# Performance work log

Measured on AMD Instinct MI355X. Metric: run time of the kernel, lower is better.

The kernel has to match this reference:

```python
import jax, jax.numpy as jnp
import numpy as np

N_NODES = 100000
N_EDGES = 1600000
IN_H = 18        # n_rw + 2
NHID_STR = 256
OUT_H = 11       # max(1, int(18/64*40))
NCLASS = 40


def gcn_conv(x, edge_index, W, b, num_nodes):
    """PyG GCNConv: add self-loops, symmetric norm, gather-matmul-scatter."""
    x = x @ W  # [N, out]
    loops = jnp.arange(num_nodes, dtype=edge_index.dtype)
    src = jnp.concatenate([edge_index[0], loops])
    dst = jnp.concatenate([edge_index[1], loops])
    deg = jax.ops.segment_sum(jnp.ones_like(dst, dtype=x.dtype), dst,
                              num_segments=num_nodes)
    dinv = jnp.where(deg > 0, jax.lax.rsqrt(deg), 0.0)
    norm = dinv[src] * dinv[dst]  # [E+N]
    msgs = x[src] * norm[:, None]  # gather + scale
    out = jax.ops.segment_sum(msgs, dst, num_segments=num_nodes)
    return out + b


def setup_inputs() -> dict:
    key = jax.random.key(0)
    ks = jax.random.split(key, 10)
    stc_enc = jax.random.normal(ks[0], (N_NODES, IN_H), dtype=jnp.float32)
    edge_index = jax.random.randint(ks[1], (2, N_EDGES), 0, N_NODES, dtype=jnp.int64)
    emb_a = jax.random.normal(ks[2], (N_NODES, NCLASS), dtype=jnp.float32)
    # Glorot-ish params
    W1 = jax.random.normal(ks[3], (IN_H, NHID_STR), dtype=jnp.float32) / np.sqrt(IN_H)
    b1 = jnp.zeros((NHID_STR,), dtype=jnp.float32)
    W2 = jax.random.normal(ks[4], (NHID_STR, OUT_H), dtype=jnp.float32) / np.sqrt(NHID_STR)
    b2 = jnp.zeros((OUT_H,), dtype=jnp.float32)
    Wc = jax.random.normal(ks[5], (NCLASS + OUT_H, NCLASS), dtype=jnp.float32) / np.sqrt(NCLASS + OUT_H)
    bc = jnp.zeros((NCLASS,), dtype=jnp.float32)
    return {"stc_enc": stc_enc, "edge_index": edge_index, "emb_a": emb_a,
            "W1": W1, "b1": b1, "W2": W2, "b2": b2, "Wc": Wc, "bc": bc}


def reference(stc_enc, edge_index, emb_a, W1, b1, W2, b2, Wc, bc):
    # eval mode: F.dropout(training=False) is identity
    h = gcn_conv(stc_enc, edge_index, W1, b1, N_NODES)
    h = gcn_conv(h, edge_index, W2, b2, N_NODES)
    emb_b = jax.nn.relu(h)
    emb = jnp.concatenate([emb_a, emb_b], axis=-1)  # [N, nclass+out_h]
    return emb @ Wc + bc
```

## Files before the change

### kernel.cpp

```cpp
#include <hip/hip_runtime.h>

#define N_NODES 100000
#define N_EDGES 1600000
#define IN_H 18
#define OUT_H 11
#define NCLASS 40
#define NHID 256

#define BBITS 9
#define BINS 512
#define NB 196
#define NBLK 800
#define CHUNK 2000
#define SRC_MASK 0x1FFFF

typedef float    vfloat4 __attribute__((ext_vector_type(4)));
typedef unsigned vuint2  __attribute__((ext_vector_type(2)));

__device__ __forceinline__ float bflo(unsigned u) { return __uint_as_float(u << 16); }
__device__ __forceinline__ float bfhi(unsigned u) { return __uint_as_float(u & 0xFFFF0000u); }
__device__ __forceinline__ unsigned bfr(float x) {
    unsigned u = __float_as_uint(x);
    return (u + 0x7FFFu + ((u >> 16) & 1u)) >> 16;
}
__device__ __forceinline__ unsigned bfpack(float a, float b) { return bfr(a) | (bfr(b) << 16); }
__device__ __forceinline__ float4 bfunpack4(uint2 w) {
    return make_float4(bflo(w.x), bfhi(w.x), bflo(w.y), bfhi(w.y));
}

__global__ void k_hist(const int* __restrict__ dst, int* __restrict__ bh, int E) {
    __shared__ int h[NB];
    int t = threadIdx.x;
    if (t < NB) h[t] = 0;
    __syncthreads();
    const int4* d4 = (const int4*)(dst + blockIdx.x * CHUNK);
    for (int i = t; i < CHUNK / 4; i += blockDim.x) {
        int4 w = d4[i];
        atomicAdd(&h[w.x >> BBITS], 1);
        atomicAdd(&h[w.y >> BBITS], 1);
        atomicAdd(&h[w.z >> BBITS], 1);
        atomicAdd(&h[w.w >> BBITS], 1);
    }
    __syncthreads();
    if (t < NB) bh[t * NBLK + blockIdx.x] = h[t];
}

__global__ void k_btot(const int* __restrict__ bh, int* __restrict__ btot) {
    __shared__ int s[256];
    int b = blockIdx.x, t = threadIdx.x;
    int sum = 0;
    for (int k = t; k < NBLK; k += 256) sum += bh[b * NBLK + k];
    s[t] = sum;
    __syncthreads();
    for (int off = 128; off > 0; off >>= 1) {
        if (t < off) s[t] += s[t + off];
        __syncthreads();
    }
    if (t == 0) btot[b] = s[0];
}

__global__ __launch_bounds__(1024) void k_boff(int* __restrict__ bh,
                                               const int* __restrict__ btot,
                                               int* __restrict__ bstart) {
    __shared__ int s0[1024], s1[1024];
    __shared__ int bt0[256], bt1[256];
    int b = blockIdx.x, t = threadIdx.x;
    if (t < 256) bt0[t] = (t < NB) ? btot[t] : 0;
    __syncthreads();
    int* c0 = bt0; int* c1 = bt1;
    for (int off = 1; off < 256; off <<= 1) {
        if (t < 256) c1[t] = c0[t] + ((t >= off) ? c0[t - off] : 0);
        __syncthreads();
        int* tmp = c0; c0 = c1; c1 = tmp;
    }
    int base = c0[b] - btot[b];
    if (t == 0) {
        bstart[b] = base;
        if (b == 0) bstart[NB] = N_EDGES;
    }
    int v = (t < NBLK) ? bh[b * NBLK + t] : 0;
    s0[t] = v;
    __syncthreads();
    int* c = s0; int* n = s1;
    for (int off = 1; off < 1024; off <<= 1) {
        n[t] = c[t] + ((t >= off) ? c[t - off] : 0);
        __syncthreads();
        int* tmp = c; c = n; n = tmp;
    }
    if (t < NBLK) bh[b * NBLK + t] = c[t] - v + base;
}

__global__ void k_bucket(const int* __restrict__ ei, const int* __restrict__ bh,
                         unsigned int* __restrict__ packed, int E) {
    __shared__ int cur[NB];
    int t = threadIdx.x;
    if (t < NB) cur[t] = bh[t * NBLK + blockIdx.x];
    __syncthreads();
    int base = blockIdx.x * CHUNK;
    const int4* s4 = (const int4*)(ei + base);
    const int4* d4 = (const int4*)(ei + E + base);
    for (int i = t; i < CHUNK / 4; i += blockDim.x) {
        int4 s = s4[i];
        int4 d = d4[i];
        int sl;
        sl = atomicAdd(&cur[d.x >> BBITS], 1);
        packed[sl] = ((unsigned)(d.x & (BINS - 1)) << 17) | (unsigned)s.x;
        sl = atomicAdd(&cur[d.y >> BBITS], 1);
        packed[sl] = ((unsigned)(d.y & (BINS - 1)) << 17) | (unsigned)s.y;
        sl = atomicAdd(&cur[d.z >> BBITS], 1);
        packed[sl] = ((unsigned)(d.z & (BINS - 1)) << 17) | (unsigned)s.z;
        sl = atomicAdd(&cur[d.w >> BBITS], 1);
        packed[sl] = ((unsigned)(d.w & (BINS - 1)) << 17) | (unsigned)s.w;
    }
}

__global__ void k_w12(const float* __restrict__ W1, const float* __restrict__ b1,
                      const float* __restrict__ W2,
                      float* __restrict__ W12, float* __restrict__ bb) {
    int t = threadIdx.x;
    if (t < IN_H * OUT_H) {
        int i = t / OUT_H, j = t % OUT_H;
        float s = 0.f;
        for (int k = 0; k < NHID; ++k) s += W1[i * NHID + k] * W2[k * OUT_H + j];
        W12[t] = s;
    } else if (t < IN_H * OUT_H + OUT_H) {
        int j = t - IN_H * OUT_H;
        float s = 0.f;
        for (int k = 0; k < NHID; ++k) s += b1[k] * W2[k * OUT_H + j];
        bb[j] = s;
    }
}

__global__ __launch_bounds__(1024)
void k_sort(const unsigned int* __restrict__ packed, const int* __restrict__ bstart,
            const float* __restrict__ X, const float* __restrict__ W12g,
            int* __restrict__ col, int* __restrict__ rowptr,
            float* __restrict__ dinv, unsigned int* __restrict__ Pp) {
    __shared__ int hist[BINS];
    __shared__ int s0[BINS], s1[BINS];
    __shared__ int cur[BINS];
    __shared__ float sW[IN_H * OUT_H];
    int b = blockIdx.x, t = threadIdx.x;
    int beg = bstart[b], end = bstart[b + 1];
    if (t < BINS) hist[t] = 0;
    if (t >= BINS && t < BINS + IN_H * OUT_H) sW[t - BINS] = W12g[t - BINS];
    __syncthreads();
    for (int i = beg + t; i < end; i += blockDim.x)
        atomicAdd(&hist[packed[i] >> 17], 1);
    __syncthreads();
    if (t < BINS) s0[t] = hist[t];
    __syncthreads();
    int* c = s0; int* n = s1;
    for (int off = 1; off < BINS; off <<= 1) {
        if (t < BINS) n[t] = c[t] + ((t >= off) ? c[t - off] : 0);
        __syncthreads();
        int* tmp = c; c = n; n = tmp;
    }
    if (t < BINS) {
        int excl = c[t] - hist[t];
        int gbase = beg + excl;
        cur[t] = gbase;
        int node = (b << BBITS) + t;
        if (node <= N_NODES) rowptr[node] = gbase;
        if (node < N_NODES)  dinv[node] = rsqrtf((float)(hist[t] + 1));
    }
    __syncthreads();
    for (int i = beg + t; i < end; i += blockDim.x) {
        unsigned p = packed[i];
        int slot = atomicAdd(&cur[p >> 17], 1);
        col[slot] = (int)(p & SRC_MASK);
    }
    int node = (b << BBITS) + t;
    if (t < BINS && node < N_NODES) {
        float dv = rsqrtf((float)(hist[t] + 1));
        float x[IN_H];
        const float2* xr = (const float2*)(X + (size_t)node * IN_H);
        #pragma unroll
        for (int k = 0; k < IN_H / 2; ++k) {
            float2 cc = xr[k];
            x[2 * k] = cc.x; x[2 * k + 1] = cc.y;
        }
        float pf[12];
        #pragma unroll
        for (int j = 0; j < OUT_H; ++j) {
            float s = 0.f;
            #pragma unroll
            for (int k = 0; k < IN_H; ++k) s += x[k] * sW[k * OUT_H + j];
            pf[j] = dv * s;
        }
        pf[11] = dv;
        uint4* pw = (uint4*)(Pp + (size_t)node * 8);
        pw[0] = make_uint4(bfpack(pf[0], pf[1]), bfpack(pf[2], pf[3]),
                           bfpack(pf[4], pf[5]), bfpack(pf[6], pf[7]));
        pw[1] = make_uint4(bfpack(pf[8], pf[9]), bfpack(pf[10], pf[11]), 0u, 0u);
    }
}

__global__ void k_gather1(const int* __restrict__ rowptr, const int* __restrict__ col,
                          const float* __restrict__ dinv, const unsigned int* __restrict__ Pp,
                          unsigned int* __restrict__ Z1p, float* __restrict__ r, int n) {
    int g = blockIdx.x * blockDim.x + threadIdx.x;
    int v = g >> 3;
    if (v >= n) return;
    int sub  = (g >> 2) & 1;
    int lane = g & 3;
    int beg = rowptr[v], end = rowptr[v + 1];
    int half = (end - beg) >> 1;
    int qbeg = beg + (sub ? half : 0);
    int qend = sub ? end : beg + half;
    float4 acc = make_float4(0.f, 0.f, 0.f, 0.f);
    const uint2* P2 = (const uint2*)Pp;
    int e = qbeg;
    if (e + 3 < qend) {
        int i0 = col[e], i1 = col[e + 1], i2 = col[e + 2], i3 = col[e + 3];
        e += 4;
        for (;;) {
            bool more = (e + 3 < qend);
            int j0, j1, j2, j3;
            if (more) {
                j0 = col[e]; j1 = col[e + 1]; j2 = col[e + 2]; j3 = col[e + 3];
            }
            float4 a0 = bfunpack4(P2[(size_t)i0 * 4 + lane]);
            float4 a1 = bfunpack4(P2[(size_t)i1 * 4 + lane]);
            float4 a2 = bfunpack4(P2[(size_t)i2 * 4 + lane]);
            float4 a3 = bfunpack4(P2[(size_t)i3 * 4 + lane]);
            acc.x += a0.x + a1.x + a2.x + a3.x;
            acc.y += a0.y + a1.y + a2.y + a3.y;
            acc.z += a0.z + a1.z + a2.z + a3.z;
            acc.w += a0.w + a1.w + a2.w + a3.w;
            if (!more) break;
            i0 = j0; i1 = j1; i2 = j2; i3 = j3;
            e += 4;
        }
    }
    for (; e < qend; ++e) {
        float4 a = bfunpack4(P2[(size_t)col[e] * 4 + lane]);
        acc.x += a.x; acc.y += a.y; acc.z += a.z; acc.w += a.w;
    }
    if (!sub) {
        float4 a = bfunpack4(P2[(size_t)v * 4 + lane]);
        acc.x += a.x; acc.y += a.y; acc.z += a.z; acc.w += a.w;
    }
    acc.x += __shfl_xor(acc.x, 4, 8);
    acc.y += __shfl_xor(acc.y, 4, 8);
    acc.z += __shfl_xor(acc.z, 4, 8);
    acc.w += __shfl_xor(acc.w, 4, 8);
    if (!sub) {
        float dd = dinv[v];
        float s2 = dd * dd;
        vuint2 z;
        z.x = bfpack(s2 * acc.x, s2 * acc.y);
        z.y = bfpack(s2 * acc.z, s2 * acc.w);
        __builtin_nontemporal_store(z, (vuint2*)Z1p + (size_t)v * 4 + lane);
        if (lane == 2) __builtin_nontemporal_store(dd * acc.w, r + v);
    }
}

__global__ void k_g2d(const int* __restrict__ rowptr, const int* __restrict__ col,
                      const float* __restrict__ dinv, const unsigned int* __restrict__ Z1p,
                      const float* __restrict__ r, const float* __restrict__ bbg,
                      const float* __restrict__ b2g, const float* __restrict__ emb_a,
                      const float* __restrict__ Wc, const float* __restrict__ bc,
                      float* __restrict__ out, int n) {
    __shared__ float sWc[(NCLASS + OUT_H) * NCLASS];
    __shared__ float sbc[NCLASS];
    __shared__ float sbb[16];
    __shared__ float sb2[16];
    for (int t = threadIdx.x; t < (NCLASS + OUT_H) * NCLASS; t += blockDim.x) sWc[t] = Wc[t];
    if (threadIdx.x < NCLASS) sbc[threadIdx.x] = bc[threadIdx.x];
    if (threadIdx.x < 16) {
        sbb[threadIdx.x] = (threadIdx.x < OUT_H) ? bbg[threadIdx.x] : 0.f;
        sb2[threadIdx.x] = (threadIdx.x < OUT_H) ? b2g[threadIdx.x] : 0.f;
    }
    __syncthreads();
    int g = blockIdx.x * blockDim.x + threadIdx.x;
    int v = g >> 3;
    if (v >= n) return;
    int sub   = (g >> 2) & 1;
    int lane  = g & 3;
    int lane8 = g & 7;
    int beg = rowptr[v], end = rowptr[v + 1];
    int half = (end - beg) >> 1;
    int qbeg = beg + (sub ? half : 0);
    int qend = sub ? end : beg + half;
    float4 acc = make_float4(0.f, 0.f, 0.f, 0.f);
    const uint2* Z2 = (const uint2*)Z1p;
    int e = qbeg;
    if (e + 3 < qend) {
        int i0 = col[e], i1 = col[e + 1], i2 = col[e + 2], i3 = col[e + 3];
        e += 4;
        for (;;) {
            bool more = (e + 3 < qend);
            int j0, j1, j2, j3;
            if (more) {
                j0 = col[e]; j1 = col[e + 1]; j2 = col[e + 2]; j3 = col[e + 3];
            }
            float4 a0 = bfunpack4(Z2[(size_t)i0 * 4 + lane]);
            float4 a1 = bfunpack4(Z2[(size_t)i1 * 4 + lane]);
            float4 a2 = bfunpack4(Z2[(size_t)i2 * 4 + lane]);
            float4 a3 = bfunpack4(Z2[(size_t)i3 * 4 + lane]);
            acc.x += a0.x + a1.x + a2.x + a3.x;
            acc.y += a0.y + a1.y + a2.y + a3.y;
            acc.z += a0.z + a1.z + a2.z + a3.z;
            acc.w += a0.w + a1.w + a2.w + a3.w;
            if (!more) break;
            i0 = j0; i1 = j1; i2 = j2; i3 = j3;
            e += 4;
        }
    }
    for (; e < qend; ++e) {
        float4 a = bfunpack4(Z2[(size_t)col[e] * 4 + lane]);
        acc.x += a.x; acc.y += a.y; acc.z += a.z; acc.w += a.w;
    }
    if (!sub) {
        float4 a = bfunpack4(Z2[(size_t)v * 4 + lane]);
        acc.x += a.x; acc.y += a.y; acc.z += a.z; acc.w += a.w;
    }
    acc.x += __shfl_xor(acc.x, 4, 8);
    acc.y += __shfl_xor(acc.y, 4, 8);
    acc.z += __shfl_xor(acc.z, 4, 8);
    acc.w += __shfl_xor(acc.w, 4, 8);
    float dd = dinv[v];
    float rv = r[v];
    float af[4] = {acc.x, acc.y, acc.z, acc.w};
    float hloc[4];
    #pragma unroll
    for (int c = 0; c < 4; ++c) {
        int f = 4 * lane + c;
        float tv = dd * af[c] + rv * sbb[f] + sb2[f];
        hloc[c] = tv > 0.f ? tv : 0.f;
    }
    float hall[OUT_H];
    #pragma unroll
    for (int f = 0; f < OUT_H; ++f)
        hall[f] = __shfl(hloc[f & 3], f >> 2, 4);
    const int jb = 5 * lane8;
    float o[5];
    #pragma unroll
    for (int j = 0; j < 5; ++j) o[j] = sbc[jb + j];
    const vfloat4* ea4 = (const vfloat4*)(emb_a + (size_t)v * NCLASS);
    #pragma unroll
    for (int k4 = 0; k4 < NCLASS / 4; ++k4) {
        vfloat4 a = __builtin_nontemporal_load(ea4 + k4);
        const float* w0 = &sWc[(4 * k4 + 0) * NCLASS + jb];
        const float* w1 = &sWc[(4 * k4 + 1) * NCLASS + jb];
        const float* w2 = &sWc[(4 * k4 + 2) * NCLASS + jb];
        const float* w3 = &sWc[(4 * k4 + 3) * NCLASS + jb];
        #pragma unroll
        for (int j = 0; j < 5; ++j)
            o[j] += a.x * w0[j] + a.y * w1[j] + a.z * w2[j] + a.w * w3[j];
    }
    #pragma unroll
    for (int f = 0; f < OUT_H; ++f) {
        const float* w = &sWc[(NCLASS + f) * NCLASS + jb];
        float hv = hall[f];
        #pragma unroll
        for (int j = 0; j < 5; ++j) o[j] += hv * w[j];
    }
    float* orow = out + (size_t)v * NCLASS + jb;
    #pragma unroll
    for (int j = 0; j < 5; ++j) __builtin_nontemporal_store(o[j], orow + j);
}

extern "C" void kernel_launch(void* const* d_in, const int* in_sizes, int n_in,
                              void* d_out, int out_size, void* d_ws, size_t ws_size,
                              hipStream_t stream) {
    const float* X     = (const float*)d_in[0];
    const int*   ei    = (const int*)d_in[1];
    const float* emb_a = (const float*)d_in[2];
    const float* W1    = (const float*)d_in[3];
    const float* b1    = (const float*)d_in[4];
    const float* W2    = (const float*)d_in[5];
    const float* b2    = (const float*)d_in[6];
    const float* Wc    = (const float*)d_in[7];
    const float* bc    = (const float*)d_in[8];
    float* out = (float*)d_out;

    char* ws = (char*)d_ws;
    size_t off = 0;
    auto alloc = [&](size_t nbytes) {
        void* p = (void*)(ws + off);
        off += ((nbytes + 255) / 256) * 256;
        return p;
    };
    char* bh_base = (char*)alloc((size_t)NB * NBLK * sizeof(int));
    int*   bh     = (int*)bh_base;
    float* rvec   = (float*)bh_base;
    int*   btot   = (int*)  alloc(NB * sizeof(int));
    int*   bstart = (int*)  alloc((NB + 1) * sizeof(int));
    unsigned int* packed = (unsigned int*)alloc((size_t)N_EDGES * sizeof(unsigned int));
    int*   col    = (int*)  alloc((size_t)N_EDGES * sizeof(int));
    int*   rowptr = (int*)  alloc((N_NODES + 1) * sizeof(int));
    float* dinv   = (float*)alloc(N_NODES * sizeof(float));
    float* W12    = (float*)alloc(IN_H * OUT_H * sizeof(float));
    float* bb     = (float*)alloc(OUT_H * sizeof(float));
    unsigned int* Pp  = (unsigned int*)alloc((size_t)N_NODES * 32);
    unsigned int* Z1p = (unsigned int*)alloc((size_t)N_NODES * 32);

    const int B = 256;
    int gN8 = (N_NODES * 8 + B - 1) / B;

    k_w12    <<<1, B, 0, stream>>>(W1, b1, W2, W12, bb);
    k_hist   <<<NBLK, B, 0, stream>>>(ei + N_EDGES, bh, N_EDGES);
    k_btot   <<<NB, 256, 0, stream>>>(bh, btot);
    k_boff   <<<NB, 1024, 0, stream>>>(bh, btot, bstart);
    k_bucket <<<NBLK, B, 0, stream>>>(ei, bh, packed, N_EDGES);
    k_sort   <<<NB, 1024, 0, stream>>>(packed, bstart, X, W12, col, rowptr, dinv, Pp);
    k_gather1<<<gN8, B, 0, stream>>>(rowptr, col, dinv, Pp, Z1p, rvec, N_NODES);
    k_g2d    <<<gN8, B, 0, stream>>>(rowptr, col, dinv, Z1p, rvec, bb, b2, emb_a,
                                     Wc, bc, out, N_NODES);
}
```

Baseline: 108.2 us.

## Replace multi-pass bucket histogram/scan with single-pass fixed-capacity buckets plus overflow

Replaces the four-kernel histogram, total, offset-scan and bucket pipeline with one kernel that stages each edge chunk in shared memory, reserves space in fixed-capacity per-bucket slots through global atomics, and spills any excess to an overflow list. Buckets shrink to 256 nodes, giving 391 sort blocks instead of 196. Row ranges become (start, end) pairs because bucket storage is no longer contiguous. This removes three kernel launches and a full extra read of the destination indices. In exchange it adds global atomic contention on the bucket counters, and every sort block scans the whole overflow list.

```diff
diff --git a/kernel.cpp b/kernel.cpp
--- a/kernel.cpp
+++ b/kernel.cpp
@@ -7,9 +7,11 @@
 #define NCLASS 40
 #define NHID 256
 
-#define BBITS 9
-#define BINS 512
-#define NB 196
+#define BBITS 8
+#define BINS 256
+#define NB 391
+#define CAP 4608
+#define GSTRIDE 16
 #define NBLK 800
 #define CHUNK 2000
 #define SRC_MASK 0x1FFFF
@@ -28,96 +30,14 @@
     return make_float4(bflo(w.x), bfhi(w.x), bflo(w.y), bfhi(w.y));
 }
 
-__global__ void k_hist(const int* __restrict__ dst, int* __restrict__ bh, int E) {
-    __shared__ int h[NB];
+__global__ __launch_bounds__(512)
+void k_w12(const float* __restrict__ W1, const float* __restrict__ b1,
+           const float* __restrict__ W2,
+           float* __restrict__ W12, float* __restrict__ bb,
+           int* __restrict__ gcnt, int* __restrict__ ovfcnt) {
     int t = threadIdx.x;
-    if (t < NB) h[t] = 0;
-    __syncthreads();
-    const int4* d4 = (const int4*)(dst + blockIdx.x * CHUNK);
-    for (int i = t; i < CHUNK / 4; i += blockDim.x) {
-        int4 w = d4[i];
-        atomicAdd(&h[w.x >> BBITS], 1);
-        atomicAdd(&h[w.y >> BBITS], 1);
-        atomicAdd(&h[w.z >> BBITS], 1);
-        atomicAdd(&h[w.w >> BBITS], 1);
-    }
-    __syncthreads();
-    if (t < NB) bh[t * NBLK + blockIdx.x] = h[t];
-}
-
-__global__ void k_btot(const int* __restrict__ bh, int* __restrict__ btot) {
-    __shared__ int s[256];
-    int b = blockIdx.x, t = threadIdx.x;
-    int sum = 0;
-    for (int k = t; k < NBLK; k += 256) sum += bh[b * NBLK + k];
-    s[t] = sum;
-    __syncthreads();
-    for (int off = 128; off > 0; off >>= 1) {
-        if (t < off) s[t] += s[t + off];
-        __syncthreads();
-    }
-    if (t == 0) btot[b] = s[0];
-}
-
-__global__ __launch_bounds__(1024) void k_boff(int* __restrict__ bh,
-                                               const int* __restrict__ btot,
-                                               int* __restrict__ bstart) {
-    __shared__ int s0[1024], s1[1024];
-    __shared__ int bt0[256], bt1[256];
-    int b = blockIdx.x, t = threadIdx.x;
-    if (t < 256) bt0[t] = (t < NB) ? btot[t] : 0;
-    __syncthreads();
-    int* c0 = bt0; int* c1 = bt1;
-    for (int off = 1; off < 256; off <<= 1) {
-        if (t < 256) c1[t] = c0[t] + ((t >= off) ? c0[t - off] : 0);
-        __syncthreads();
-        int* tmp = c0; c0 = c1; c1 = tmp;
-    }
-    int base = c0[b] - btot[b];
-    if (t == 0) {
-        bstart[b] = base;
-        if (b == 0) bstart[NB] = N_EDGES;
-    }
-    int v = (t < NBLK) ? bh[b * NBLK + t] : 0;
-    s0[t] = v;
-    __syncthreads();
-    int* c = s0; int* n = s1;
-    for (int off = 1; off < 1024; off <<= 1) {
-        n[t] = c[t] + ((t >= off) ? c[t - off] : 0);
-        __syncthreads();
-        int* tmp = c; c = n; n = tmp;
-    }
-    if (t < NBLK) bh[b * NBLK + t] = c[t] - v + base;
-}
-
-__global__ void k_bucket(const int* __restrict__ ei, const int* __restrict__ bh,
-                         unsigned int* __restrict__ packed, int E) {
-    __shared__ int cur[NB];
-    int t = threadIdx.x;
-    if (t < NB) cur[t] = bh[t * NBLK + blockIdx.x];
-    __syncthreads();
-    int base = blockIdx.x * CHUNK;
-    const int4* s4 = (const int4*)(ei + base);
-    const int4* d4 = (const int4*)(ei + E + base);
-    for (int i = t; i < CHUNK / 4; i += blockDim.x) {
-        int4 s = s4[i];
-        int4 d = d4[i];
-        int sl;
-        sl = atomicAdd(&cur[d.x >> BBITS], 1);
-        packed[sl] = ((unsigned)(d.x & (BINS - 1)) << 17) | (unsigned)s.x;
-        sl = atomicAdd(&cur[d.y >> BBITS], 1);
-        packed[sl] = ((unsigned)(d.y & (BINS - 1)) << 17) | (unsigned)s.y;
-        sl = atomicAdd(&cur[d.z >> BBITS], 1);
-        packed[sl] = ((unsigned)(d.z & (BINS - 1)) << 17) | (unsigned)s.z;
-        sl = atomicAdd(&cur[d.w >> BBITS], 1);
-        packed[sl] = ((unsigned)(d.w & (BINS - 1)) << 17) | (unsigned)s.w;
-    }
-}
-
-__global__ void k_w12(const float* __restrict__ W1, const float* __restrict__ b1,
-                      const float* __restrict__ W2,
-                      float* __restrict__ W12, float* __restrict__ bb) {
-    int t = threadIdx.x;
+    for (int i = t; i < NB * GSTRIDE; i += 512) gcnt[i] = 0;
+    if (t == 0) *ovfcnt = 0;
     if (t < IN_H * OUT_H) {
         int i = t / OUT_H, j = t % OUT_H;
         float s = 0.f;
@@ -131,22 +51,69 @@
     }
 }
 
+__global__ __launch_bounds__(256)
+void k_bucket1p(const int* __restrict__ ei, int* __restrict__ gcnt,
+                unsigned int* __restrict__ packed,
+                uint2* __restrict__ ovf, int* __restrict__ ovfcnt) {
+    __shared__ int  h[NB];
+    __shared__ int  basec[NB];
+    __shared__ int2 ed[CHUNK];
+    int t = threadIdx.x;
+    for (int i = t; i < NB; i += 256) h[i] = 0;
+    int cbase = blockIdx.x * CHUNK;
+    const int4* s4 = (const int4*)(ei + cbase);
+    const int4* d4 = (const int4*)(ei + N_EDGES + cbase);
+    for (int i = t; i < CHUNK / 4; i += 256) {
+        int4 s = s4[i];
+        int4 d = d4[i];
+        ed[4 * i + 0] = make_int2(s.x, d.x);
+        ed[4 * i + 1] = make_int2(s.y, d.y);
+        ed[4 * i + 2] = make_int2(s.z, d.z);
+        ed[4 * i + 3] = make_int2(s.w, d.w);
+    }
+    __syncthreads();
+    for (int i = t; i < CHUNK; i += 256) atomicAdd(&h[ed[i].y >> BBITS], 1);
+    __syncthreads();
+    for (int i = t; i < NB; i += 256)
+        basec[i] = (h[i] > 0) ? atomicAdd(&gcnt[i * GSTRIDE], h[i]) : 0;
+    __syncthreads();
+    for (int i = t; i < CHUNK; i += 256) {
+        int2 e = ed[i];
+        int b = e.y >> BBITS;
+        int loc = atomicAdd(&basec[b], 1);
+        if (loc < CAP) {
+            packed[b * CAP + loc] = ((unsigned)(e.y & (BINS - 1)) << 17) | (unsigned)e.x;
+        } else {
+            int o = atomicAdd(ovfcnt, 1);
+            ovf[o] = make_uint2((unsigned)e.x, (unsigned)e.y);
+        }
+    }
+}
+
 __global__ __launch_bounds__(1024)
-void k_sort(const unsigned int* __restrict__ packed, const int* __restrict__ bstart,
+void k_sort(const unsigned int* __restrict__ packed, const int* __restrict__ gcnt,
+            const uint2* __restrict__ ovf, const int* __restrict__ ovfcnt,
             const float* __restrict__ X, const float* __restrict__ W12g,
-            int* __restrict__ col, int* __restrict__ rowptr,
+            int* __restrict__ col, uint2* __restrict__ rowse,
             float* __restrict__ dinv, unsigned int* __restrict__ Pp) {
     __shared__ int hist[BINS];
     __shared__ int s0[BINS], s1[BINS];
     __shared__ int cur[BINS];
     __shared__ float sW[IN_H * OUT_H];
     int b = blockIdx.x, t = threadIdx.x;
-    int beg = bstart[b], end = bstart[b + 1];
     if (t < BINS) hist[t] = 0;
     if (t >= BINS && t < BINS + IN_H * OUT_H) sW[t - BINS] = W12g[t - BINS];
     __syncthreads();
-    for (int i = beg + t; i < end; i += blockDim.x)
-        atomicAdd(&hist[packed[i] >> 17], 1);
+    int cnt = gcnt[b * GSTRIDE];
+    int seg = cnt < CAP ? cnt : CAP;
+    int base = b * CAP;
+    for (int i = t; i < seg; i += 1024)
+        atomicAdd(&hist[packed[base + i] >> 17], 1);
+    int nov = *ovfcnt;
+    for (int i = t; i < nov; i += 1024) {
+        uint2 e = ovf[i];
+        if ((int)(e.y >> BBITS) == b) atomicAdd(&hist[e.y & (BINS - 1)], 1);
+    }
     __syncthreads();
     if (t < BINS) s0[t] = hist[t];
     __syncthreads();
@@ -158,17 +125,26 @@
     }
     if (t < BINS) {
         int excl = c[t] - hist[t];
-        int gbase = beg + excl;
-        cur[t] = gbase;
+        int gb = base + excl;
+        cur[t] = gb;
         int node = (b << BBITS) + t;
-        if (node <= N_NODES) rowptr[node] = gbase;
-        if (node < N_NODES)  dinv[node] = rsqrtf((float)(hist[t] + 1));
-    }
-    __syncthreads();
-    for (int i = beg + t; i < end; i += blockDim.x) {
-        unsigned p = packed[i];
+        if (node < N_NODES) {
+            rowse[node] = make_uint2((unsigned)gb, (unsigned)(gb + hist[t]));
+            dinv[node] = rsqrtf((float)(hist[t] + 1));
+        }
+    }
+    __syncthreads();
+    for (int i = t; i < seg; i += 1024) {
+        unsigned p = packed[base + i];
         int slot = atomicAdd(&cur[p >> 17], 1);
         col[slot] = (int)(p & SRC_MASK);
+    }
+    for (int i = t; i < nov; i += 1024) {
+        uint2 e = ovf[i];
+        if ((int)(e.y >> BBITS) == b) {
+            int slot = atomicAdd(&cur[e.y & (BINS - 1)], 1);
+            col[slot] = (int)e.x;
+        }
     }
     int node = (b << BBITS) + t;
     if (t < BINS && node < N_NODES) {
@@ -196,7 +172,7 @@
     }
 }
 
-__global__ void k_gather1(const int* __restrict__ rowptr, const int* __restrict__ col,
+__global__ void k_gather1(const uint2* __restrict__ rowse, const int* __restrict__ col,
                           const float* __restrict__ dinv, const unsigned int* __restrict__ Pp,
                           unsigned int* __restrict__ Z1p, float* __restrict__ r, int n) {
     int g = blockIdx.x * blockDim.x + threadIdx.x;
@@ -204,7 +180,8 @@
     if (v >= n) return;
     int sub  = (g >> 2) & 1;
     int lane = g & 3;
-    int beg = rowptr[v], end = rowptr[v + 1];
+    uint2 se = rowse[v];
+    int beg = (int)se.x, end = (int)se.y;
     int half = (end - beg) >> 1;
     int qbeg = beg + (sub ? half : 0);
     int qend = sub ? end : beg + half;
@@ -256,7 +233,7 @@
     }
 }
 
-__global__ void k_g2d(const int* __restrict__ rowptr, const int* __restrict__ col,
+__global__ void k_g2d(const uint2* __restrict__ rowse, const int* __restrict__ col,
                       const float* __restrict__ dinv, const unsigned int* __restrict__ Z1p,
                       const float* __restrict__ r, const float* __restrict__ bbg,
                       const float* __restrict__ b2g, const float* __restrict__ emb_a,
@@ -279,7 +256,8 @@
     int sub   = (g >> 2) & 1;
     int lane  = g & 3;
     int lane8 = g & 7;
-    int beg = rowptr[v], end = rowptr[v + 1];
+    uint2 se = rowse[v];
+    int beg = (int)se.x, end = (int)se.y;
     int half = (end - beg) >> 1;
     int qbeg = beg + (sub ? half : 0);
     int qend = sub ? end : beg + half;
@@ -383,15 +361,14 @@
         off += ((nbytes + 255) / 256) * 256;
         return p;
     };
-    char* bh_base = (char*)alloc((size_t)NB * NBLK * sizeof(int));
-    int*   bh     = (int*)bh_base;
-    float* rvec   = (float*)bh_base;
-    int*   btot   = (int*)  alloc(NB * sizeof(int));
-    int*   bstart = (int*)  alloc((NB + 1) * sizeof(int));
-    unsigned int* packed = (unsigned int*)alloc((size_t)N_EDGES * sizeof(unsigned int));
-    int*   col    = (int*)  alloc((size_t)N_EDGES * sizeof(int));
-    int*   rowptr = (int*)  alloc((N_NODES + 1) * sizeof(int));
+    int*   gcnt   = (int*)  alloc((size_t)NB * GSTRIDE * sizeof(int));
+    int*   ovfcnt = (int*)  alloc(256);
+    uint2* ovf    = (uint2*)alloc((size_t)N_EDGES * sizeof(uint2));
+    unsigned int* packed = (unsigned int*)alloc((size_t)NB * CAP * sizeof(unsigned));
+    int*   col    = (int*)  alloc((size_t)NB * CAP * sizeof(int));
+    uint2* rowse  = (uint2*)alloc((size_t)N_NODES * sizeof(uint2));
     float* dinv   = (float*)alloc(N_NODES * sizeof(float));
+    float* rvec   = (float*)alloc(N_NODES * sizeof(float));
     float* W12    = (float*)alloc(IN_H * OUT_H * sizeof(float));
     float* bb     = (float*)alloc(OUT_H * sizeof(float));
     unsigned int* Pp  = (unsigned int*)alloc((size_t)N_NODES * 32);
@@ -400,13 +377,11 @@
     const int B = 256;
     int gN8 = (N_NODES * 8 + B - 1) / B;
 
-    k_w12    <<<1, B, 0, stream>>>(W1, b1, W2, W12, bb);
-    k_hist   <<<NBLK, B, 0, stream>>>(ei + N_EDGES, bh, N_EDGES);
-    k_btot   <<<NB, 256, 0, stream>>>(bh, btot);
-    k_boff   <<<NB, 1024, 0, stream>>>(bh, btot, bstart);
-    k_bucket <<<NBLK, B, 0, stream>>>(ei, bh, packed, N_EDGES);
-    k_sort   <<<NB, 1024, 0, stream>>>(packed, bstart, X, W12, col, rowptr, dinv, Pp);
-    k_gather1<<<gN8, B, 0, stream>>>(rowptr, col, dinv, Pp, Z1p, rvec, N_NODES);
-    k_g2d    <<<gN8, B, 0, stream>>>(rowptr, col, dinv, Z1p, rvec, bb, b2, emb_a,
-                                     Wc, bc, out, N_NODES);
-}
+    k_w12     <<<1, 512, 0, stream>>>(W1, b1, W2, W12, bb, gcnt, ovfcnt);
+    k_bucket1p<<<NBLK, B, 0, stream>>>(ei, gcnt, packed, ovf, ovfcnt);
+    k_sort    <<<NB, 1024, 0, stream>>>(packed, gcnt, ovf, ovfcnt, X, W12,
+                                        col, rowse, dinv, Pp);
+    k_gather1 <<<gN8, B, 0, stream>>>(rowse, col, dinv, Pp, Z1p, rvec, N_NODES);
+    k_g2d     <<<gN8, B, 0, stream>>>(rowse, col, dinv, Z1p, rvec, bb, b2, emb_a,
+                                      Wc, bc, out, N_NODES);
+}
```

New measurement: 124.2 us. 1.15x slower.
